# Kernel tuning notes

Hardware: AMD Instinct MI355X
Metric: run time of the kernel (lower is better)

The kernel has to match this reference:

```python
import jax, jax.numpy as jnp
import numpy as np

NUM_HEADS = 16
HEAD_DIM = 128
HIDDEN = 2048
C_KV = 512
C_Q = 1024
ROPE_DIM = 64
BATCH = 2
SEQ = 2048
ROPE_BASE = 10000.0


def _rope_cos_sin(seq_len, dim, dtype):
    # standard RoPE tables: [seq, dim] with concatenated (half, half) freqs
    inv_freq = 1.0 / (ROPE_BASE ** (jnp.arange(0, dim, 2, dtype=jnp.float32) / dim))
    t = jnp.arange(seq_len, dtype=jnp.float32)
    freqs = jnp.outer(t, inv_freq)                      # [S, dim/2]
    emb = jnp.concatenate([freqs, freqs], axis=-1)      # [S, dim]
    return jnp.cos(emb).astype(dtype), jnp.sin(emb).astype(dtype)


def _rotate_half(x):
    x1, x2 = jnp.split(x, 2, axis=-1)
    return jnp.concatenate([-x2, x1], axis=-1)


def _apply_rope(x, cos, sin):
    # x: [B, S, H, D]; cos/sin: [S, D] -> broadcast over batch and heads
    c = cos[None, :, None, :]
    s = sin[None, :, None, :]
    return x * c + _rotate_half(x) * s


def setup_inputs() -> dict:
    key = jax.random.key(0)
    ks = jax.random.split(key, 10)

    def xavier(k, shape):
        fan_in, fan_out = shape
        limit = np.sqrt(6.0 / (fan_in + fan_out))
        return jax.random.uniform(k, shape, jnp.float32, -limit, limit)

    hidden_states = jax.random.normal(ks[0], (BATCH, SEQ, HIDDEN), jnp.float32)
    # causal mask: 1 = masked out (positions j > i)
    causal = jnp.triu(jnp.ones((SEQ, SEQ), jnp.int32), k=1)
    mask = jnp.broadcast_to(causal[None, None], (BATCH, 1, SEQ, SEQ))
    return {
        "hidden_states": hidden_states,
        "mask": mask,
        "W_DKV": xavier(ks[1], (HIDDEN, C_KV)),
        "W_UK": xavier(ks[2], (C_KV, NUM_HEADS * HEAD_DIM)),
        "W_UV": xavier(ks[3], (C_KV, NUM_HEADS * HEAD_DIM)),
        "W_DQ": xavier(ks[4], (HIDDEN, C_Q)),
        "W_UQ": xavier(ks[5], (C_Q, NUM_HEADS * HEAD_DIM)),
        "W_QR": xavier(ks[6], (C_Q, NUM_HEADS * ROPE_DIM)),
        "W_KR": xavier(ks[7], (HIDDEN, ROPE_DIM)),
        "W_O": xavier(ks[8], (NUM_HEADS * HEAD_DIM, HIDDEN)),
    }


def reference(hidden_states, mask, W_DKV, W_UK, W_UV, W_DQ, W_UQ, W_QR, W_KR, W_O):
    B, S, _ = hidden_states.shape
    scale = 1.0 / jnp.sqrt(jnp.float32(HEAD_DIM + ROPE_DIM))

    c_KV = hidden_states @ W_DKV                         # [B,S,c_kv]
    k_C = (c_KV @ W_UK).reshape(B, S, NUM_HEADS, HEAD_DIM)
    v = (c_KV @ W_UV).reshape(B, S, NUM_HEADS, HEAD_DIM)
    c_Q = hidden_states @ W_DQ                           # [B,S,c_q]
    q_C = (c_Q @ W_UQ).reshape(B, S, NUM_HEADS, HEAD_DIM)
    q_R = (c_Q @ W_QR).reshape(B, S, NUM_HEADS, ROPE_DIM)
    k_R = (hidden_states @ W_KR).reshape(B, S, 1, ROPE_DIM)

    cos, sin = _rope_cos_sin(S, ROPE_DIM, hidden_states.dtype)
    q_R = _apply_rope(q_R, cos, sin)
    k_R = _apply_rope(k_R, cos, sin)
    k_R = jnp.broadcast_to(k_R, (B, S, NUM_HEADS, ROPE_DIM))

    q = jnp.concatenate([q_C, q_R], axis=-1)             # [B,S,H,D+R]
    k = jnp.concatenate([k_C, k_R], axis=-1)             # [B,S,H,D+R]

    scores = jnp.einsum('bqhd,bkhd->bhqk', q, k) * scale
    scores = scores + mask.astype(scores.dtype) * jnp.asarray(-1e9, scores.dtype)
    probs = jax.nn.softmax(scores, axis=-1)
    out = jnp.einsum('bhqk,bkhd->bqhd', probs, v).reshape(B, S, NUM_HEADS * HEAD_DIM)
    return out @ W_O
```

## Files before the change

### kernel.cpp

```cpp
#include <hip/hip_runtime.h>
#include <hip/hip_bf16.h>

typedef __bf16 bf16x8 __attribute__((ext_vector_type(8)));
typedef float f32x4 __attribute__((ext_vector_type(4)));
typedef float f32x16 __attribute__((ext_vector_type(16)));
using BF = __hip_bfloat16;

constexpr int B_   = 2;
constexpr int S_   = 2048;
constexpr int NH_  = 16;
constexpr int HD_  = 128;
constexpr int HID_ = 2048;
constexpr int CKV_ = 512;
constexpr int CQ_  = 1024;
constexpr int RD_  = 64;
constexpr int M_   = B_ * S_;
constexpr int DQK_ = HD_ + RD_;

__device__ __forceinline__ f32x4 mfma16(bf16x8 a, bf16x8 b, f32x4 c) {
  return __builtin_amdgcn_mfma_f32_16x16x32_bf16(a, b, c, 0, 0, 0);
}
__device__ __forceinline__ f32x16 mfma32(bf16x8 a, bf16x8 b, f32x16 c) {
  return __builtin_amdgcn_mfma_f32_32x32x16_bf16(a, b, c, 0, 0, 0);
}
__device__ __forceinline__ unsigned cvtpk(float a, float b) {
  unsigned r;
  asm("v_cvt_pk_bf16_f32 %0, %1, %2" : "=v"(r) : "v"(a), "v"(b));
  return r;
}
__device__ __forceinline__ void gload16(const void* g, void* lds) {
  __builtin_amdgcn_global_load_lds((const __attribute__((address_space(1))) void*)g,
                                   (__attribute__((address_space(3))) void*)lds,
                                   16, 0, 0);
}
__device__ __forceinline__ void plswap(unsigned& x, unsigned& y, bool hi) {
#if __has_builtin(__builtin_amdgcn_permlane32_swap)
  typedef unsigned u32x2 __attribute__((ext_vector_type(2)));
  u32x2 r = __builtin_amdgcn_permlane32_swap(x, y, false, false);
  x = r[0];
  y = r[1];
#else
  unsigned sx = (unsigned)__shfl_xor((int)x, 32, 64);
  unsigned sy = (unsigned)__shfl_xor((int)y, 32, 64);
  unsigned nx = hi ? sy : x;
  unsigned ny = hi ? y : sx;
  x = nx;
  y = ny;
#endif
}

__global__ __launch_bounds__(256) void f2b_kern(const float* __restrict__ in,
                                                BF* __restrict__ out, int n4) {
  int i = blockIdx.x * 256 + threadIdx.x;
  if (i >= n4) return;
  float4 v = reinterpret_cast<const float4*>(in)[i];
  BF o[4] = {__float2bfloat16(v.x), __float2bfloat16(v.y),
             __float2bfloat16(v.z), __float2bfloat16(v.w)};
  reinterpret_cast<uint2*>(out)[i] = *reinterpret_cast<uint2*>(o);
}

__global__ __launch_bounds__(256) void wtrans_all(const float* __restrict__ w0,
                                                  const float* __restrict__ w1,
                                                  const float* __restrict__ w2,
                                                  const float* __restrict__ w3,
                                                  const float* __restrict__ w4,
                                                  const float* __restrict__ w5,
                                                  const float* __restrict__ w6,
                                                  const float* __restrict__ w7,
                                                  BF* __restrict__ tCat1,
                                                  BF* __restrict__ tCat2,
                                                  BF* __restrict__ tCat3,
                                                  BF* __restrict__ tWO) {
  const int cum[9] = {0, 1024, 3072, 3328, 4352, 5376, 7424, 8448, 12544};
  const int nxt[8] = {16, 32, 4, 64, 64, 64, 32, 64};
  const int Kt[8]  = {2048, 2048, 2048, 512, 512, 1024, 1024, 2048};
  const int Nt[8]  = {512, 1024, 64, 2048, 2048, 2048, 1024, 2048};
  int bid = blockIdx.x;
  int j = 0;
#pragma unroll
  for (int t = 1; t < 8; t++)
    if (bid >= cum[t]) j = t;
  const float* in = (j == 0) ? w0 : (j == 1) ? w1 : (j == 2) ? w2 : (j == 3) ? w3
                   : (j == 4) ? w4 : (j == 5) ? w5 : (j == 6) ? w6 : w7;
  BF* out = (j == 0) ? tCat1 : (j == 1) ? tCat1 + (size_t)512 * 2048
           : (j == 2) ? tCat1 + (size_t)1536 * 2048
           : (j == 3) ? tCat2 : (j == 4) ? tCat2 + (size_t)2048 * 512
           : (j == 5) ? tCat3 : (j == 6) ? tCat3 + (size_t)2048 * 1024 : tWO;
  const int K = Kt[j], N = Nt[j];
  int rem = bid - cum[j];
  int bx = rem % nxt[j], by = rem / nxt[j];
  int n0 = bx * 32, k0 = by * 32;

  __shared__ float t[32][33];
  int tx = threadIdx.x, ty = threadIdx.y;
#pragma unroll
  for (int j4 = 0; j4 < 4; j4++) {
    int k = k0 + ty + j4 * 8, n = n0 + tx;
    t[ty + j4 * 8][tx] = (n < N) ? in[(size_t)k * N + n] : 0.f;
  }
  __syncthreads();
#pragma unroll
  for (int j4 = 0; j4 < 4; j4++) {
    int n = n0 + ty + j4 * 8, k = k0 + tx;
    out[(size_t)n * K + k] = __float2bfloat16(t[tx][ty + j4 * 8]);
  }
}

template <int F>
__global__ __launch_bounds__(256) void gemm_f(const BF* __restrict__ A,
                                              const BF* __restrict__ Bt,
                                              void* __restrict__ C0,
                                              void* __restrict__ C1,
                                              void* __restrict__ C2,
                                              int M, int N, int K) {
  __shared__ BF As[2][128][32];
  __shared__ BF Bs[2][128][32];
  const int tid = threadIdx.x;
  const int w = tid >> 6, l = tid & 63;
  const int lr = l & 15, lg = l >> 4;
  const int wr = w >> 1, wc = w & 1;
  const int gx = gridDim.x;
  const int nwg = gx * gridDim.y;
  const int f = blockIdx.y * gx + blockIdx.x;
  const int swz = (f & 7) * (nwg >> 3) + (f >> 3);
  const int m0 = (swz / gx) * 128, n0 = (swz % gx) * 128;

  f32x4 acc[4][4];
#pragma unroll
  for (int m = 0; m < 4; m++)
#pragma unroll
    for (int n = 0; n < 4; n++) acc[m][n] = (f32x4){0.f, 0.f, 0.f, 0.f};

  auto STAGE = [&](int buf, int k0) {
#pragma unroll
    for (int j = 0; j < 2; j++) {
      int idx = tid + j * 256;
      int row = idx >> 2, seg = idx & 3;
      gload16(A + (size_t)(m0 + row) * K + k0 + seg * 8, &As[buf][0][0] + idx * 8);
      gload16(Bt + (size_t)(n0 + row) * K + k0 + seg * 8, &Bs[buf][0][0] + idx * 8);
    }
  };

  STAGE(0, 0);
  __syncthreads();
  const int nk = K >> 5;
  for (int ki = 0; ki < nk; ki++) {
    const int cur = ki & 1;
    if (ki + 1 < nk) STAGE(cur ^ 1, (ki + 1) << 5);
    __builtin_amdgcn_sched_barrier(0);
    bf16x8 af[4], bfr[4];
#pragma unroll
    for (int m = 0; m < 4; m++)
      af[m] = *reinterpret_cast<const bf16x8*>(&As[cur][wr * 64 + m * 16 + lr][lg * 8]);
#pragma unroll
    for (int n = 0; n < 4; n++)
      bfr[n] = *reinterpret_cast<const bf16x8*>(&Bs[cur][wc * 64 + n * 16 + lr][lg * 8]);
#pragma unroll
    for (int m = 0; m < 4; m++)
#pragma unroll
      for (int n = 0; n < 4; n++) acc[m][n] = mfma16(af[m], bfr[n], acc[m][n]);
    __syncthreads();
  }

#pragma unroll
  for (int m = 0; m < 4; m++) {
#pragma unroll
    for (int n = 0; n < 4; n++) {
#pragma unroll
      for (int j = 0; j < 4; j++) {
        int row = m0 + wr * 64 + m * 16 + lg * 4 + j;
        int col = n0 + wc * 64 + n * 16 + lr;
        float v = acc[m][n][j];
        if constexpr (F == 1) {
          if (col < 512)
            ((BF*)C0)[(size_t)row * 512 + col] = __float2bfloat16(v);
          else if (col < 1536)
            ((BF*)C1)[(size_t)row * 1024 + (col - 512)] = __float2bfloat16(v);
          else
            ((BF*)C2)[(size_t)row * 128 + (col - 1536)] = __float2bfloat16(v);
        } else {
          ((float*)C0)[(size_t)row * 2048 + col] = v;
        }
      }
    }
  }
}

__global__ __launch_bounds__(256) void gemm_f23(const BF* __restrict__ cQ,
                                                const BF* __restrict__ t3,
                                                BF* __restrict__ qbuf,
                                                BF* __restrict__ qRt,
                                                const BF* __restrict__ cKV,
                                                const BF* __restrict__ t2,
                                                BF* __restrict__ kbuf,
                                                BF* __restrict__ vTb) {
  __shared__ BF As[2][128][32];
  __shared__ BF Bs[2][128][32];
  const int tid = threadIdx.x;
  const int w = tid >> 6, l = tid & 63;
  const int lr = l & 15, lg = l >> 4;
  const int wr = w >> 1, wc = w & 1;
  const int f = blockIdx.y * 56 + blockIdx.x;
  const int swz = (f & 7) * (1792 >> 3) + (f >> 3);
  const int xt = swz % 56;
  const int m0 = (swz / 56) * 128;
  const bool isF3 = xt < 24;
  const BF* A  = isF3 ? cQ : cKV;
  const BF* Bt = isF3 ? t3 : t2;
  const int K  = isF3 ? 1024 : 512;
  const int n0 = (isF3 ? xt : xt - 24) * 128;

  f32x4 acc[4][4];
#pragma unroll
  for (int m = 0; m < 4; m++)
#pragma unroll
    for (int n = 0; n < 4; n++) acc[m][n] = (f32x4){0.f, 0.f, 0.f, 0.f};

  auto STAGE = [&](int buf, int k0) {
#pragma unroll
    for (int j = 0; j < 2; j++) {
      int idx = tid + j * 256;
      int row = idx >> 2, seg = idx & 3;
      gload16(A + (size_t)(m0 + row) * K + k0 + seg * 8, &As[buf][0][0] + idx * 8);
      gload16(Bt + (size_t)(n0 + row) * K + k0 + seg * 8, &Bs[buf][0][0] + idx * 8);
    }
  };

  STAGE(0, 0);
  __syncthreads();
  const int nk = K >> 5;
  for (int ki = 0; ki < nk; ki++) {
    const int cur = ki & 1;
    if (ki + 1 < nk) STAGE(cur ^ 1, (ki + 1) << 5);
    __builtin_amdgcn_sched_barrier(0);
    bf16x8 af[4], bfr[4];
#pragma unroll
    for (int m = 0; m < 4; m++)
      af[m] = *reinterpret_cast<const bf16x8*>(&As[cur][wr * 64 + m * 16 + lr][lg * 8]);
#pragma unroll
    for (int n = 0; n < 4; n++)
      bfr[n] = *reinterpret_cast<const bf16x8*>(&Bs[cur][wc * 64 + n * 16 + lr][lg * 8]);
#pragma unroll
    for (int m = 0; m < 4; m++)
#pragma unroll
      for (int n = 0; n < 4; n++) acc[m][n] = mfma16(af[m], bfr[n], acc[m][n]);
    __syncthreads();
  }

#pragma unroll
  for (int m = 0; m < 4; m++) {
#pragma unroll
    for (int n = 0; n < 4; n++) {
#pragma unroll
      for (int j = 0; j < 4; j++) {
        int row = m0 + wr * 64 + m * 16 + lg * 4 + j;
        int col = n0 + wc * 64 + n * 16 + lr;
        float v = acc[m][n][j];
        int b = row >> 11, s = row & 2047;
        if (isF3) {
          if (col < 2048) {
            int h = col >> 7, d = col & 127;
            qbuf[((size_t)(b * 16 + h) * 2048 + s) * 192 + d] = __float2bfloat16(v);
          } else {
            qRt[(size_t)row * 1024 + (col - 2048)] = __float2bfloat16(v);
          }
        } else {
          if (col < 2048) {
            int h = col >> 7, d = col & 127;
            kbuf[((size_t)(b * 16 + h) * 2048 + s) * 192 + d] = __float2bfloat16(v);
          } else {
            int c2 = col - 2048, h = c2 >> 7, d = c2 & 127;
            vTb[((size_t)(b * 16 + h) * 128 + d) * 2048 + s] = __float2bfloat16(v);
          }
        }
      }
    }
  }
}

__global__ __launch_bounds__(256) void rope_q(const BF* __restrict__ qr, BF* __restrict__ qb) {
  int idx = blockIdx.x * 256 + threadIdx.x;
  int d = idx & 63, h = (idx >> 6) & 15, m = idx >> 10;
  int s = m & 2047, b = m >> 11;
  float x = __bfloat162float(qr[(size_t)(m << 10) + (h << 6) + d]);
  float other = __bfloat162float(qr[(size_t)(m << 10) + (h << 6) + (d ^ 32)]);
  float rot = (d < 32) ? -other : other;
  int di = d & 31;
  float arg = (float)s * powf(10000.f, -(float)di / 32.0f);
  float c = cosf(arg), sn = sinf(arg);
  qb[((size_t)(b * 16 + h) * 2048 + s) * 192 + 128 + d] = __float2bfloat16(x * c + rot * sn);
}

__global__ __launch_bounds__(256) void rope_k(const BF* __restrict__ kr, BF* __restrict__ kb) {
  int idx = blockIdx.x * 256 + threadIdx.x;
  int d = idx & 63, m = idx >> 6;
  int s = m & 2047, b = m >> 11;
  float x = __bfloat162float(kr[(size_t)m * 128 + d]);
  float other = __bfloat162float(kr[(size_t)m * 128 + (d ^ 32)]);
  float rot = (d < 32) ? -other : other;
  int di = d & 31;
  float arg = (float)s * powf(10000.f, -(float)di / 32.0f);
  float val = x * cosf(arg) + rot * sinf(arg);
  BF v = __float2bfloat16(val);
#pragma unroll
  for (int h = 0; h < 16; h++)
    kb[((size_t)(b * 16 + h) * 2048 + s) * 192 + 128 + d] = v;
}

__global__ __launch_bounds__(256, 2) void attn_kern(const BF* __restrict__ qb,
                                                    const BF* __restrict__ kb,
                                                    const BF* __restrict__ vT,
                                                    BF* __restrict__ o) {
  const int yy = blockIdx.y;
  const bool second = yy >= 16;
  const int bh = second ? ((yy - 16) * 2 + 1) : (yy * 2);
  const int qt = second ? (int)blockIdx.x : (15 - (int)blockIdx.x);
  const int q0 = qt * 128;
  const int tid = threadIdx.x;
  const int w = tid >> 6, l = tid & 63;
  const int lo5 = l & 31;
  const int hi = l >> 5;
  const int l7 = l & 7;

  __shared__ __align__(16) char smem[81920];

  const int q = q0 + w * 32 + lo5;
  const int qmax = q0 + w * 32 + 31;

  bf16x8 aq[12];
  {
    const BF* qrow = qb + ((size_t)bh * 2048 + q) * 192;
#pragma unroll
    for (int kst = 0; kst < 12; kst++)
      aq[kst] = *reinterpret_cast<const bf16x8*>(qrow + kst * 16 + hi * 8);
  }

  f32x16 Oacc[4];
#pragma unroll
  for (int dt = 0; dt < 4; dt++)
#pragma unroll
    for (int r = 0; r < 16; r++) Oacc[dt][r] = 0.f;
  float mrow = -3e38f, lrow = 0.f;

  const float scale = 0.07216878364870323f;
  const int nch = (q0 + 128) >> 6;

  auto STAGE = [&](int buf, int ch) {
    const int cc = ch << 6;
    BF* Ks = (BF*)(smem + buf * 40960);
    BF* Vs = (BF*)(smem + buf * 40960 + 24576);
#pragma unroll
    for (int j2 = 0; j2 < 6; j2++) {
      int D = tid + j2 * 256;
      int row = D / 24, sp = D % 24;
      int sl = sp ^ (row & 7);
      gload16(kb + ((size_t)bh * 2048 + cc + row) * 192 + sl * 8, Ks + D * 8);
    }
#pragma unroll
    for (int j2 = 0; j2 < 4; j2++) {
      int D = tid + j2 * 256;
      int row = D >> 3, sp = D & 7;
      int sl = sp ^ (row & 7);
      gload16(vT + ((size_t)bh * 128 + row) * 2048 + cc + sl * 8, Vs + D * 8);
    }
  };

  STAGE(0, 0);
  __syncthreads();

  for (int ch = 0; ch < nch; ch++) {
    const int c0 = ch << 6;
    const int cur = ch & 1;
    if (ch + 1 < nch) STAGE(cur ^ 1, ch + 1);
    __builtin_amdgcn_sched_barrier(0);
    BF* Ks = (BF*)(smem + cur * 40960);
    BF* Vs = (BF*)(smem + cur * 40960 + 24576);

    f32x16 sf[2];
    __builtin_amdgcn_s_setprio(1);
#pragma unroll
    for (int t = 0; t < 2; t++) {
      if (c0 + t * 32 <= qmax) {
        f32x16 a0, a1;
#pragma unroll
        for (int r = 0; r < 16; r++) { a0[r] = 0.f; a1[r] = 0.f; }
#pragma unroll
        for (int kst = 0; kst < 12; kst++) {
          bf16x8 kfr = *reinterpret_cast<const bf16x8*>(
              Ks + (t * 32 + lo5) * 192 + (((kst * 2 + hi) ^ l7) * 8));
          if (kst & 1) a1 = mfma32(kfr, aq[kst], a1);
          else         a0 = mfma32(kfr, aq[kst], a0);
        }
        sf[t] = a0 + a1;
      } else {
#pragma unroll
        for (int r = 0; r < 16; r++) sf[t][r] = 0.f;
      }
    }
    __builtin_amdgcn_s_setprio(0);

    float mx = -3e38f;
#pragma unroll
    for (int t = 0; t < 2; t++) {
#pragma unroll
      for (int r = 0; r < 16; r++) {
        int key = c0 + t * 32 + (r & 3) + 8 * (r >> 2) + 4 * hi;
        float v = sf[t][r] * scale;
        v = (key <= q) ? v : -1e30f;
        sf[t][r] = v;
        mx = fmaxf(mx, v);
      }
    }
    mx = fmaxf(mx, __shfl_xor(mx, 32, 64));
    float mnew = fmaxf(mrow, mx);
    float corr = __expf(mrow - mnew);
    mrow = mnew;
    float psum = 0.f;
#pragma unroll
    for (int t = 0; t < 2; t++)
#pragma unroll
      for (int r = 0; r < 16; r++) {
        float p = __expf(sf[t][r] - mnew);
        sf[t][r] = p;
        psum += p;
      }
    psum += __shfl_xor(psum, 32, 64);
    lrow = lrow * corr + psum;
#pragma unroll
    for (int dt = 0; dt < 4; dt++) Oacc[dt] *= corr;

    bf16x8 pb[4];
#pragma unroll
    for (int ks = 0; ks < 4; ks++) {
      if (c0 + ks * 16 > qmax) continue;
      int t = ks >> 1, base = (ks & 1) * 8;
      unsigned Xa = cvtpk(sf[t][base + 0], sf[t][base + 1]);
      unsigned Xb = cvtpk(sf[t][base + 2], sf[t][base + 3]);
      unsigned Ya = cvtpk(sf[t][base + 4], sf[t][base + 5]);
      unsigned Yb = cvtpk(sf[t][base + 6], sf[t][base + 7]);
      plswap(Xa, Ya, hi != 0);
      plswap(Xb, Yb, hi != 0);
      union { unsigned u[4]; bf16x8 v; } pk_;
      pk_.u[0] = Xa; pk_.u[1] = Xb; pk_.u[2] = Ya; pk_.u[3] = Yb;
      pb[ks] = pk_.v;
    }

    __builtin_amdgcn_s_setprio(1);
#pragma unroll
    for (int ks = 0; ks < 4; ks++) {
      if (c0 + ks * 16 > qmax) continue;
#pragma unroll
      for (int dt = 0; dt < 4; dt++) {
        bf16x8 vfr = *reinterpret_cast<const bf16x8*>(
            Vs + (dt * 32 + lo5) * 64 + (((ks * 2 + hi) ^ l7) * 8));
        Oacc[dt] = mfma32(vfr, pb[ks], Oacc[dt]);
      }
    }
    __builtin_amdgcn_s_setprio(0);
    __syncthreads();
  }

  BF* Osh = (BF*)smem;
  float rinv = 1.0f / lrow;
  const int orow = w * 32 + lo5;
#pragma unroll
  for (int dt = 0; dt < 4; dt++) {
#pragma unroll
    for (int g = 0; g < 4; g++) {
      unsigned d0 = cvtpk(Oacc[dt][g * 4 + 0] * rinv, Oacc[dt][g * 4 + 1] * rinv);
      unsigned d1 = cvtpk(Oacc[dt][g * 4 + 2] * rinv, Oacc[dt][g * 4 + 3] * rinv);
      uint2 pr; pr.x = d0; pr.y = d1;
      *reinterpret_cast<uint2*>(Osh + orow * 136 + dt * 32 + g * 8 + hi * 4) = pr;
    }
  }
  __syncthreads();
  const int b = bh >> 4, h = bh & 15;
  const int cb = tid & 15, rb = tid >> 4;
#pragma unroll
  for (int rr = 0; rr < 8; rr++) {
    int row = rb + rr * 16;
    bf16x8 v = *reinterpret_cast<const bf16x8*>(Osh + row * 136 + cb * 8);
    *reinterpret_cast<bf16x8*>(o + ((size_t)(b * 2048 + q0 + row)) * 2048 + h * 128 + cb * 8) = v;
  }
}

extern "C" void kernel_launch(void* const* d_in, const int* in_sizes, int n_in,
                              void* d_out, int out_size, void* d_ws, size_t ws_size,
                              hipStream_t stream) {
  const float* hs   = (const float*)d_in[0];
  const float* wDKV = (const float*)d_in[2];
  const float* wUK  = (const float*)d_in[3];
  const float* wUV  = (const float*)d_in[4];
  const float* wDQ  = (const float*)d_in[5];
  const float* wUQ  = (const float*)d_in[6];
  const float* wQR  = (const float*)d_in[7];
  const float* wKR  = (const float*)d_in[8];
  const float* wO   = (const float*)d_in[9];
  float* out = (float*)d_out;

  char* ws = (char*)d_ws;
  size_t off = 0;
  auto alloc = [&](size_t bytes) -> char* {
    char* p = ws + off;
    off += (bytes + 255) & ~(size_t)255;
    return p;
  };
  BF* hsb   = (BF*)alloc((size_t)M_ * HID_ * 2);
  BF* tCat1 = (BF*)alloc((size_t)1664 * HID_ * 2);
  BF* tCat2 = (BF*)alloc((size_t)4096 * CKV_ * 2);
  BF* tCat3 = (BF*)alloc((size_t)3072 * CQ_ * 2);
  BF* tWO   = (BF*)alloc((size_t)HID_ * (NH_*HD_) * 2);
  BF* cKV   = (BF*)alloc((size_t)M_ * CKV_ * 2);
  BF* cQ    = (BF*)alloc((size_t)M_ * CQ_ * 2);
  BF* qbuf  = (BF*)alloc((size_t)B_ * NH_ * S_ * DQK_ * 2);
  BF* kbuf  = (BF*)alloc((size_t)B_ * NH_ * S_ * DQK_ * 2);
  BF* vTb   = (BF*)alloc((size_t)B_ * NH_ * HD_ * S_ * 2);
  BF* qRt   = (BF*)alloc((size_t)M_ * (NH_*RD_) * 2);
  BF* kRt   = (BF*)alloc((size_t)M_ * 128 * 2);
  BF* aout  = (BF*)alloc((size_t)M_ * (NH_*HD_) * 2);

  f2b_kern<<<(M_ * HID_ / 4 + 255) / 256, 256, 0, stream>>>(hs, hsb, M_ * HID_ / 4);

  wtrans_all<<<12544, dim3(32, 8), 0, stream>>>(wDKV, wDQ, wKR, wUK, wUV, wUQ, wQR, wO,
                                                tCat1, tCat2, tCat3, tWO);

  gemm_f<1><<<dim3(1664 / 128, M_ / 128), 256, 0, stream>>>(hsb, tCat1, cKV, cQ, kRt, M_, 1664, HID_);
  gemm_f23<<<dim3(56, M_ / 128), 256, 0, stream>>>(cQ, tCat3, qbuf, qRt, cKV, tCat2, kbuf, vTb);

  rope_q<<<(M_ * NH_ * RD_) / 256, 256, 0, stream>>>(qRt, qbuf);
  rope_k<<<(M_ * RD_) / 256, 256, 0, stream>>>(kRt, kbuf);

  attn_kern<<<dim3(S_ / 128, B_ * NH_), 256, 0, stream>>>(qbuf, kbuf, vTb, aout);

  gemm_f<4><<<dim3(2048 / 128, M_ / 128), 256, 0, stream>>>(aout, tWO, out, nullptr, nullptr, M_, 2048, HID_);
}
```

Before: 328.7 us.

## Triple-buffer GEMM shared-memory tiles with fine-grained vmcnt waits

Both projection GEMM kernels move from double to triple buffering of the A/B tiles in LDS. Global loads now run two k-steps ahead, and the full __syncthreads is replaced by a partial s_waitcnt vmcnt plus s_barrier, so loads stay in flight across iterations. Wave priority is also raised around the MFMA block. This aims to hide global-load latency, at the cost of more LDS per block (possibly lower occupancy) and fragile hand-written wait counts.

Result: faster. 316.2 us (-3.8%).

```diff
diff --git a/kernel.cpp b/kernel.cpp
--- a/kernel.cpp
+++ b/kernel.cpp
@@ -113,8 +113,8 @@
                                               void* __restrict__ C1,
                                               void* __restrict__ C2,
                                               int M, int N, int K) {
-  __shared__ BF As[2][128][32];
-  __shared__ BF Bs[2][128][32];
+  __shared__ BF As[3][128][32];
+  __shared__ BF Bs[3][128][32];
   const int tid = threadIdx.x;
   const int w = tid >> 6, l = tid & 63;
   const int lr = l & 15, lg = l >> 4;
@@ -141,13 +141,15 @@
     }
   };
 
+  const int nk = K >> 5;
   STAGE(0, 0);
-  __syncthreads();
-  const int nk = K >> 5;
+  if (nk > 1) STAGE(1, 32);
+  asm volatile("s_waitcnt vmcnt(4)" ::: "memory");
+  __builtin_amdgcn_sched_barrier(0);
+  __builtin_amdgcn_s_barrier();
+
+  int cur = 0;
   for (int ki = 0; ki < nk; ki++) {
-    const int cur = ki & 1;
-    if (ki + 1 < nk) STAGE(cur ^ 1, (ki + 1) << 5);
-    __builtin_amdgcn_sched_barrier(0);
     bf16x8 af[4], bfr[4];
 #pragma unroll
     for (int m = 0; m < 4; m++)
@@ -155,11 +157,28 @@
 #pragma unroll
     for (int n = 0; n < 4; n++)
       bfr[n] = *reinterpret_cast<const bf16x8*>(&Bs[cur][wc * 64 + n * 16 + lr][lg * 8]);
+    if (ki + 2 < nk) {
+      int nb = cur + 2; if (nb >= 3) nb -= 3;
+      STAGE(nb, (ki + 2) << 5);
+    }
+    __builtin_amdgcn_sched_barrier(0);
+    __builtin_amdgcn_s_setprio(1);
 #pragma unroll
     for (int m = 0; m < 4; m++)
 #pragma unroll
       for (int n = 0; n < 4; n++) acc[m][n] = mfma16(af[m], bfr[n], acc[m][n]);
-    __syncthreads();
+    __builtin_amdgcn_s_setprio(0);
+    __builtin_amdgcn_sched_barrier(0);
+    if (ki + 1 < nk) {
+      if (ki + 2 < nk) {
+        asm volatile("s_waitcnt vmcnt(4)" ::: "memory");
+      } else {
+        asm volatile("s_waitcnt vmcnt(0)" ::: "memory");
+      }
+      __builtin_amdgcn_sched_barrier(0);
+      __builtin_amdgcn_s_barrier();
+    }
+    cur = cur + 1; if (cur >= 3) cur = 0;
   }
 
 #pragma unroll
@@ -194,8 +213,8 @@
                                                 const BF* __restrict__ t2,
                                                 BF* __restrict__ kbuf,
                                                 BF* __restrict__ vTb) {
-  __shared__ BF As[2][128][32];
-  __shared__ BF Bs[2][128][32];
+  __shared__ BF As[3][128][32];
+  __shared__ BF Bs[3][128][32];
   const int tid = threadIdx.x;
   const int w = tid >> 6, l = tid & 63;
   const int lr = l & 15, lg = l >> 4;
@@ -226,13 +245,15 @@
     }
   };
 
+  const int nk = K >> 5;
   STAGE(0, 0);
-  __syncthreads();
-  const int nk = K >> 5;
+  STAGE(1, 32);
+  asm volatile("s_waitcnt vmcnt(4)" ::: "memory");
+  __builtin_amdgcn_sched_barrier(0);
+  __builtin_amdgcn_s_barrier();
+
+  int cur = 0;
   for (int ki = 0; ki < nk; ki++) {
-    const int cur = ki & 1;
-    if (ki + 1 < nk) STAGE(cur ^ 1, (ki + 1) << 5);
-    __builtin_amdgcn_sched_barrier(0);
     bf16x8 af[4], bfr[4];
 #pragma unroll
     for (int m = 0; m < 4; m++)
@@ -240,11 +261,28 @@
 #pragma unroll
     for (int n = 0; n < 4; n++)
       bfr[n] = *reinterpret_cast<const bf16x8*>(&Bs[cur][wc * 64 + n * 16 + lr][lg * 8]);
+    if (ki + 2 < nk) {
+      int nb = cur + 2; if (nb >= 3) nb -= 3;
+      STAGE(nb, (ki + 2) << 5);
+    }
+    __builtin_amdgcn_sched_barrier(0);
+    __builtin_amdgcn_s_setprio(1);
 #pragma unroll
     for (int m = 0; m < 4; m++)
 #pragma unroll
       for (int n = 0; n < 4; n++) acc[m][n] = mfma16(af[m], bfr[n], acc[m][n]);
-    __syncthreads();
+    __builtin_amdgcn_s_setprio(0);
+    __builtin_amdgcn_sched_barrier(0);
+    if (ki + 1 < nk) {
+      if (ki + 2 < nk) {
+        asm volatile("s_waitcnt vmcnt(4)" ::: "memory");
+      } else {
+        asm volatile("s_waitcnt vmcnt(0)" ::: "memory");
+      }
+      __builtin_amdgcn_sched_barrier(0);
+      __builtin_amdgcn_s_barrier();
+    }
+    cur = cur + 1; if (cur >= 3) cur = 0;
   }
 
 #pragma unroll
```
